# Performance work log

Measured on AMD Instinct MI355X. Metric: run time of the kernel, lower is better.

The kernel has to match this reference:

```python
import jax, jax.numpy as jnp
import numpy as np

MODEL_SIZE = 512
HEADS = 8
T = 2048
B = 2


def setup_inputs() -> dict:
    key = jax.random.key(0)
    ks = jax.random.split(key, 10)
    E = MODEL_SIZE
    w = 0.02  # weight init scale for numerical stability
    return {
        "input": jax.random.normal(ks[0], (T, B, E), jnp.float32),
        "pos": jax.random.normal(ks[1], (T, 1, E), jnp.float32),
        "in_proj_weight": jax.random.normal(ks[2], (3 * E, E), jnp.float32) * w,
        "out_proj_weight": jax.random.normal(ks[3], (E, E), jnp.float32) * w,
        "pos_proj_weight": jax.random.normal(ks[4], (E, E), jnp.float32) * w,
        "in_proj_bias": jax.random.normal(ks[5], (3 * E,), jnp.float32) * w,
        "out_proj_bias": jax.random.normal(ks[6], (E,), jnp.float32) * w,
        "pos_proj_bias": jax.random.normal(ks[7], (E,), jnp.float32) * w,
        "r_w_bias": jax.random.normal(ks[8], (HEADS, E // HEADS), jnp.float32) * w,
        "r_r_bias": jax.random.normal(ks[9], (HEADS, E // HEADS), jnp.float32) * w,
    }


def _rel_shift(x):
    # x: [B, H, T, R] -> Transformer-XL relative shift
    b, h, t, r = x.shape
    x = jnp.pad(x, ((0, 0), (0, 0), (0, 0), (1, 0)))  # [B,H,T,R+1]
    x = x.reshape(b, h, r + 1, t)[:, :, 1:, :]        # drop first row
    return x.reshape(b, h, t, r)


def reference(input, pos, in_proj_weight, out_proj_weight, pos_proj_weight,
              in_proj_bias, out_proj_bias, pos_proj_bias, r_w_bias, r_r_bias):
    t, b, e = input.shape
    h = r_w_bias.shape[0]
    d = e // h
    scale = 1.0 / np.sqrt(d).astype(np.float32)

    # fused QKV projection (time-first layout [T,B,E])
    qkv = input @ in_proj_weight.T + in_proj_bias          # [T,B,3E]
    q, k, v = jnp.split(qkv, 3, axis=-1)
    q = q.reshape(t, b, h, d)
    k = k.reshape(t, b, h, d)
    v = v.reshape(t, b, h, d)

    # relative position projection (pos batch dim is 1)
    r = (pos[:, 0] @ pos_proj_weight.T + pos_proj_bias).reshape(-1, h, d)  # [R,H,D]

    # content (AC) and position (BD) scores
    ac = jnp.einsum('tbhd,sbhd->bhts', q + r_w_bias, k)    # [B,H,T,T]
    bd = jnp.einsum('tbhd,rhd->bhtr', q + r_r_bias, r)     # [B,H,T,R]
    bd = _rel_shift(bd)[..., :t]

    attn = jax.nn.softmax((ac + bd) * scale, axis=-1)      # [B,H,T,T]
    ctx = jnp.einsum('bhts,sbhd->tbhd', attn, v).reshape(t, b, e)
    return ctx @ out_proj_weight.T + out_proj_bias
```

## Files before the change

kernel.cpp:

```cpp
#include <hip/hip_runtime.h>

#define T_SEQ 2048
#define BATCH 2
#define HEADS 8
#define DHEAD 64
#define EMB   512

typedef __attribute__((ext_vector_type(8))) short short8;
typedef __attribute__((ext_vector_type(4))) float floatx4;
typedef __attribute__((ext_vector_type(8))) unsigned short ushort8;
typedef __attribute__((ext_vector_type(4))) unsigned short ushort4v;

__device__ __forceinline__ unsigned short f2b(float f) {
    union { float f; unsigned u; } v; v.f = f;
    unsigned r = v.u + 0x7fffu + ((v.u >> 16) & 1u);
    return (unsigned short)(r >> 16);
}
__device__ __forceinline__ unsigned short f2bt(float f) {
    union { float f; unsigned u; } v; v.f = f;
    return (unsigned short)(v.u >> 16);
}
__device__ __forceinline__ float b2f(unsigned short s) {
    union { unsigned u; float f; } v; v.u = ((unsigned)s) << 16; return v.f;
}
__device__ __forceinline__ short8 ld_frag(const unsigned short* p) {
    ushort4v lo = *(const ushort4v*)p;
    ushort4v hi = *(const ushort4v*)(p + 4);
    short8 r;
    r[0] = lo[0]; r[1] = lo[1]; r[2] = lo[2]; r[3] = lo[3];
    r[4] = hi[0]; r[5] = hi[1]; r[6] = hi[2]; r[7] = hi[3];
    return r;
}
__device__ __forceinline__ void st8(unsigned short* p, ushort8 v) {
    ushort4v lo = { v[0], v[1], v[2], v[3] };
    ushort4v hi = { v[4], v[5], v[6], v[7] };
    *(ushort4v*)p = lo;
    *(ushort4v*)(p + 4) = hi;
}
#define MFMA16(a, b, c) __builtin_amdgcn_mfma_f32_16x16x32_bf16(a, b, c, 0, 0, 0)

__global__ __launch_bounds__(256)
void cvt_all(const float* __restrict__ s0, const float* __restrict__ s1,
             const float* __restrict__ s2, const float* __restrict__ s3,
             const float* __restrict__ s4,
             unsigned short* __restrict__ d0, unsigned short* __restrict__ d1,
             unsigned short* __restrict__ d2, unsigned short* __restrict__ d3,
             unsigned short* __restrict__ d4)
{
    const int i = blockIdx.x * 256 + threadIdx.x;
    const float* s; unsigned short* d; int off;
    if      (i <  524288) { s = s0; d = d0; off = i; }
    else if (i <  786432) { s = s1; d = d1; off = i -  524288; }
    else if (i <  983040) { s = s2; d = d2; off = i -  786432; }
    else if (i < 1048576) { s = s3; d = d3; off = i -  983040; }
    else if (i < 1114112) { s = s4; d = d4; off = i - 1048576; }
    else return;
    const float4 v = ((const float4*)s)[off];
    ushort4v o = { f2b(v.x), f2b(v.y), f2b(v.z), f2b(v.w) };
    ((ushort4v*)d)[off] = o;
}

template<int MODE>
__global__ __launch_bounds__(256)
void gemm_bf16(const unsigned short* __restrict__ A, const unsigned short* __restrict__ B,
               const float* __restrict__ bias, void* __restrict__ out0,
               void* __restrict__ out1, void* __restrict__ out2, int K)
{
    __shared__ unsigned short As[128 * 36];
    __shared__ unsigned short Bs[128 * 36];
    const int bm  = blockIdx.y * 128;
    const int bn  = blockIdx.x * 128;
    const int tid = threadIdx.x;
    const int lane = tid & 63, w = tid >> 6;
    const int m16 = lane & 15, quad = lane >> 4;
    const int wm = (w & 1) * 64, wn = (w >> 1) * 64;

    floatx4 acc[4][4];
    #pragma unroll
    for (int i = 0; i < 4; ++i)
        #pragma unroll
        for (int j = 0; j < 4; ++j) acc[i][j] = (floatx4){0.f, 0.f, 0.f, 0.f};

    for (int k0 = 0; k0 < K; k0 += 32) {
        #pragma unroll
        for (int s = tid; s < 512; s += 256) {
            const int row = s >> 2, c = (s & 3) * 8;
            *(ushort8*)&As[row * 36 + c] = *(const ushort8*)(A + (size_t)(bm + row) * K + k0 + c);
            *(ushort8*)&Bs[row * 36 + c] = *(const ushort8*)(B + (size_t)(bn + row) * K + k0 + c);
        }
        __syncthreads();
        short8 af[4], bf[4];
        #pragma unroll
        for (int f = 0; f < 4; ++f) {
            af[f] = ld_frag(&As[(wm + f * 16 + m16) * 36 + quad * 8]);
            bf[f] = ld_frag(&Bs[(wn + f * 16 + m16) * 36 + quad * 8]);
        }
        #pragma unroll
        for (int fm = 0; fm < 4; ++fm)
            #pragma unroll
            for (int fn = 0; fn < 4; ++fn)
                acc[fm][fn] = MFMA16(af[fm], bf[fn], acc[fm][fn]);
        __syncthreads();
    }

    #pragma unroll
    for (int fn = 0; fn < 4; ++fn) {
        const int n = bn + wn + fn * 16 + m16;
        const float bv = bias[n];
        #pragma unroll
        for (int fm = 0; fm < 4; ++fm) {
            #pragma unroll
            for (int rgi = 0; rgi < 4; ++rgi) {
                const int m = bm + wm + fm * 16 + quad * 4 + rgi;
                const float val = acc[fm][fn][rgi] + bv;
                if (MODE == 0) {
                    const int t = m >> 1, b = m & 1;
                    const int reg = n >> 9, c = n & 511, h = c >> 6, dd = c & 63;
                    unsigned short* dst = (unsigned short*)(reg == 0 ? out0 : (reg == 1 ? out1 : out2));
                    dst[((size_t)(b * HEADS + h) * T_SEQ + t) * DHEAD + dd] = f2b(val);
                } else if (MODE == 1) {
                    ((unsigned short*)out0)[(size_t)m * EMB + n] = f2b(val);
                } else {
                    ((float*)out0)[(size_t)m * EMB + n] = val;
                }
            }
        }
    }
}

__global__ __launch_bounds__(256)
void transpose_v(const unsigned short* __restrict__ v_s, unsigned short* __restrict__ vT)
{
    __shared__ unsigned short tile[64 * 68];
    const int t0 = blockIdx.x * 64, bh = blockIdx.y;
    const int tid = threadIdx.x;
    const unsigned short* src = v_s + ((size_t)bh * T_SEQ + t0) * DHEAD;
    #pragma unroll
    for (int s = tid; s < 512; s += 256) {
        const int row = s >> 3, c = (s & 7) * 8;
        st8(&tile[row * 68 + c], *(const ushort8*)(src + row * DHEAD + c));
    }
    __syncthreads();
    unsigned short* dst = vT + (size_t)bh * DHEAD * T_SEQ + t0;
    #pragma unroll
    for (int s = tid; s < 512; s += 256) {
        const int d = s >> 3, c = (s & 7) * 8;
        ushort8 o;
        #pragma unroll
        for (int j = 0; j < 8; ++j) o[j] = tile[(c + j) * 68 + d];
        *(ushort8*)(dst + (size_t)d * T_SEQ + c) = o;
    }
}

__global__ __launch_bounds__(256)
void attn_mfma(const unsigned short* __restrict__ qg_, const unsigned short* __restrict__ kg_,
               const unsigned short* __restrict__ vtg_, const unsigned short* __restrict__ rg_,
               const float* __restrict__ rwb, const float* __restrict__ rrb,
               unsigned short* __restrict__ ctx)
{
    const int T   = T_SEQ;
    const int tb  = blockIdx.x;
    const int t0  = tb * 64;
    const int bh  = blockIdx.y;
    const int h   = bh & 7;
    const int b   = bh >> 3;
    const int tid = threadIdx.x;
    const int lane = tid & 63;
    const int w    = tid >> 6;
    const int m16  = lane & 15;
    const int quad = lane >> 4;
    const int ibase = 16 * w + quad * 4;

    __shared__ unsigned short lds[34624];
    unsigned short* ring  = lds + 26112;
    unsigned short* qrw_s = lds;
    unsigned short* qrr_s = lds + 8704;

    const unsigned short* qg  = qg_  + ((size_t)bh * T + t0) * DHEAD;
    const unsigned short* kg  = kg_  + (size_t)bh * T * DHEAD;
    const unsigned short* vtg = vtg_ + (size_t)bh * DHEAD * T;
    const unsigned short* rg  = rg_  + h * DHEAD;

    const float QSCALE = 0.125f * 1.44269504089f;
    for (int idx = tid; idx < 65 * 16; idx += 256) {
        const int row = idx >> 4, c = (idx & 15) << 2;
        ushort4v qv = {0, 0, 0, 0};
        if (t0 + row < T) qv = *(const ushort4v*)(qg + row * DHEAD + c);
        const float4 rr = *(const float4*)(rrb + h * DHEAD + c);
        qrr_s[row * 68 + c + 0] = f2b((b2f(qv[0]) + rr.x) * QSCALE);
        qrr_s[row * 68 + c + 1] = f2b((b2f(qv[1]) + rr.y) * QSCALE);
        qrr_s[row * 68 + c + 2] = f2b((b2f(qv[2]) + rr.z) * QSCALE);
        qrr_s[row * 68 + c + 3] = f2b((b2f(qv[3]) + rr.w) * QSCALE);
        if (row < 64) {
            const float4 rw = *(const float4*)(rwb + h * DHEAD + c);
            qrw_s[row * 68 + c + 0] = f2b((b2f(qv[0]) + rw.x) * QSCALE);
            qrw_s[row * 68 + c + 1] = f2b((b2f(qv[1]) + rw.y) * QSCALE);
            qrw_s[row * 68 + c + 2] = f2b((b2f(qv[2]) + rw.z) * QSCALE);
            qrw_s[row * 68 + c + 3] = f2b((b2f(qv[3]) + rw.w) * QSCALE);
        }
    }
    __syncthreads();

    short8 a_ac[2], a_qrl[2], a_qru[2];
    {
        const unsigned short* p0 = &qrw_s[(16 * w + m16) * 68 + quad * 8];
        a_ac[0]  = ld_frag(p0);  a_ac[1]  = ld_frag(p0 + 32);
        const unsigned short* p1 = &qrr_s[(16 * w + m16) * 68 + quad * 8];
        a_qrl[0] = ld_frag(p1);  a_qrl[1] = ld_frag(p1 + 32);
        const unsigned short* p2 = &qrr_s[(16 * w + 1 + m16) * 68 + quad * 8];
        a_qru[0] = ld_frag(p2);  a_qru[1] = ld_frag(p2 + 32);
    }

    const int srow0 = tid >> 3,          scol0 = (tid & 7) * 8;
    const int srow1 = (tid + 256) >> 3,  scol1 = (tid & 7) * 8;

    ushort8 kr[2], vr[2], rr8[2];
    auto prefetch = [&](int s0n) {
        const bool ln = (s0n <= t0);
        const int jb = (ln ? (s0n + T - t0 - 64) : (s0n - t0 - 65)) + 64;
        int j0 = jb + srow0; j0 = j0 < 0 ? 0 : (j0 > T - 1 ? T - 1 : j0);
        int j1 = jb + srow1; j1 = j1 < 0 ? 0 : (j1 > T - 1 ? T - 1 : j1);
        kr[0]  = *(const ushort8*)(kg + (size_t)(s0n + srow0) * DHEAD + scol0);
        kr[1]  = *(const ushort8*)(kg + (size_t)(s0n + srow1) * DHEAD + scol1);
        vr[0]  = *(const ushort8*)(vtg + (size_t)srow0 * T + s0n + scol0);
        vr[1]  = *(const ushort8*)(vtg + (size_t)srow1 * T + s0n + scol1);
        rr8[0] = *(const ushort8*)(rg + (size_t)j0 * EMB + scol0);
        rr8[1] = *(const ushort8*)(rg + (size_t)j1 * EMB + scol1);
    };
    auto store_bufs = [&](int q) {
        unsigned short* kb = lds + q * 4352;
        unsigned short* vb = lds + 8704 + q * 4352;
        unsigned short* rb = lds + 17408 + q * 4352;
        st8(&kb[srow0 * 68 + scol0], kr[0]);
        st8(&kb[srow1 * 68 + scol1], kr[1]);
        st8(&vb[srow0 * 68 + scol0], vr[0]);
        st8(&vb[srow1 * 68 + scol1], vr[1]);
        st8(&rb[srow0 * 68 + scol0], rr8[0]);
        st8(&rb[srow1 * 68 + scol1], rr8[1]);
    };
    auto stage_to = [&](unsigned short* dstb, int jbase) {
        #pragma unroll
        for (int idx = tid; idx < 512; idx += 256) {
            const int row = idx >> 3, c = (idx & 7) * 8;
            int j = jbase + row; j = j < 0 ? 0 : (j > T - 1 ? T - 1 : j);
            st8(&dstb[row * 68 + c], *(const ushort8*)(rg + (size_t)j * EMB + c));
        }
    };
    auto qr_half = [&](const unsigned short* rsb, const short8* aq, int slotbase) {
        #pragma unroll
        for (int cc = 0; cc < 4; ++cc) {
            floatx4 q4 = (floatx4){0.f, 0.f, 0.f, 0.f};
            #pragma unroll
            for (int ks = 0; ks < 2; ++ks) {
                short8 bfr = ld_frag(&rsb[(16 * cc + m16) * 68 + ks * 32 + quad * 8]);
                q4 = MFMA16(aq[ks], bfr, q4);
            }
            #pragma unroll
            for (int rgi = 0; rgi < 4; ++rgi)
                ring[(ibase + rgi) * 133 + slotbase + 16 * cc + m16] = f2bt(q4[rgi]);
        }
    };

    floatx4 O[4];
    float lrun[4];
    #pragma unroll
    for (int ct = 0; ct < 4; ++ct) O[ct] = (floatx4){0.f, 0.f, 0.f, 0.f};
    #pragma unroll
    for (int rgi = 0; rgi < 4; ++rgi) lrun[rgi] = 0.f;

    {
        stage_to(lds + 17408 + 4352, T - t0 - 64);
        prefetch(0);
        __syncthreads();
        qr_half(lds + 17408 + 4352, a_qrl, 0);
        store_bufs(0);
        __syncthreads();
    }

    for (int na = 0; na < T / 64; ++na) {
        const int s0 = na * 64;
        const int p = na & 1;
        unsigned short* kb = lds + p * 4352;
        unsigned short* vb = lds + 8704 + p * 4352;
        unsigned short* rp = lds + 17408 + p * 4352;
        const bool lower = (s0 <= t0);
        const int nph    = lower ? (s0 >> 6) : ((s0 - t0) >> 6);
        const int rbase  = (nph & 1) * 64;
        const int wbase  = 64 - rbase;
        const bool hasNext = (na + 1 < T / 64);

        floatx4 acf[4];
        #pragma unroll
        for (int ct = 0; ct < 4; ++ct) {
            acf[ct] = (floatx4){0.f, 0.f, 0.f, 0.f};
            #pragma unroll
            for (int ks = 0; ks < 2; ++ks) {
                short8 bfr = ld_frag(&kb[(16 * ct + m16) * 68 + ks * 32 + quad * 8]);
                acf[ct] = MFMA16(a_ac[ks], bfr, acf[ct]);
            }
        }
        qr_half(rp, lower ? a_qrl : a_qru, wbase);
        if (hasNext) prefetch(s0 + 64);
        __syncthreads();

        if (s0 != t0) {
            #pragma unroll
            for (int ct = 0; ct < 4; ++ct) {
                #pragma unroll
                for (int rgi = 0; rgi < 4; ++rgi) {
                    const int i = ibase + rgi;
                    const int slot = ((63 - i + 16 * ct + m16) + rbase) & 127;
                    acf[ct][rgi] += b2f(ring[i * 133 + slot]);
                }
            }
            if (s0 == t0 + 64 && lane == 48 && w == 3)
                acf[0][3] -= b2f(ring[63 * 133 + (rbase & 127)]);
        } else {
            #pragma unroll
            for (int ct = 0; ct < 4; ++ct) {
                #pragma unroll
                for (int rgi = 0; rgi < 4; ++rgi) {
                    const int i = ibase + rgi, u = 16 * ct + m16;
                    if (u <= i) acf[ct][rgi] += b2f(ring[i * 133 + (((63 - i + u) + rbase) & 127)]);
                }
            }
            unsigned short* rpo = lds + 17408 + (1 - p) * 4352;
            __syncthreads();
            stage_to(rpo, -1);
            __syncthreads();
            qr_half(rpo, a_qru, 64);
            __syncthreads();
            #pragma unroll
            for (int ct = 0; ct < 4; ++ct) {
                #pragma unroll
                for (int rgi = 0; rgi < 4; ++rgi) {
                    const int i = ibase + rgi, u = 16 * ct + m16;
                    if (u >= i + 2) acf[ct][rgi] += b2f(ring[i * 133 + 63 - i + u]);
                }
            }
        }

        #pragma unroll
        for (int rgi = 0; rgi < 4; ++rgi) {
            #pragma unroll
            for (int ct = 0; ct < 4; ++ct) {
                const float pv = exp2f(acf[ct][rgi]);
                acf[ct][rgi] = pv;
                lrun[rgi] += pv;
            }
        }
        #pragma unroll
        for (int ct = 0; ct < 4; ++ct)
            #pragma unroll
            for (int rgi = 0; rgi < 4; ++rgi)
                rp[(ibase + rgi) * 68 + 16 * ct + m16] = f2bt(acf[ct][rgi]);
        if (hasNext) store_bufs(1 - p);
        __syncthreads();

        short8 ap[2];
        {
            const unsigned short* pp = &rp[(16 * w + m16) * 68 + quad * 8];
            ap[0] = ld_frag(pp); ap[1] = ld_frag(pp + 32);
        }
        #pragma unroll
        for (int ct = 0; ct < 4; ++ct) {
            #pragma unroll
            for (int ks = 0; ks < 2; ++ks) {
                short8 bfr = ld_frag(&vb[(16 * ct + m16) * 68 + ks * 32 + quad * 8]);
                O[ct] = MFMA16(ap[ks], bfr, O[ct]);
            }
        }
    }

    #pragma unroll
    for (int rgi = 0; rgi < 4; ++rgi) {
        float l = lrun[rgi];
        #pragma unroll
        for (int off = 1; off < 16; off <<= 1)
            l += __shfl_xor(l, off);
        const float inv = 1.f / l;
        const int t = t0 + ibase + rgi;
        #pragma unroll
        for (int ct = 0; ct < 4; ++ct)
            ctx[((size_t)t * BATCH + b) * EMB + h * DHEAD + 16 * ct + m16] = f2bt(O[ct][rgi] * inv);
    }
}

extern "C" void kernel_launch(void* const* d_in, const int* in_sizes, int n_in,
                              void* d_out, int out_size, void* d_ws, size_t ws_size,
                              hipStream_t stream)
{
    const float* input = (const float*)d_in[0];
    const float* pos   = (const float*)d_in[1];
    const float* w_in  = (const float*)d_in[2];
    const float* w_out = (const float*)d_in[3];
    const float* w_pos = (const float*)d_in[4];
    const float* b_in  = (const float*)d_in[5];
    const float* b_out = (const float*)d_in[6];
    const float* b_pos = (const float*)d_in[7];
    const float* rwb   = (const float*)d_in[8];
    const float* rrb   = (const float*)d_in[9];

    unsigned short* ws     = (unsigned short*)d_ws;
    unsigned short* inb    = ws;
    unsigned short* posb   = ws + 2097152;
    unsigned short* w_inb  = ws + 3145728;
    unsigned short* w_posb = ws + 3932160;
    unsigned short* v_s    = ws + 4194304;
    unsigned short* w_outb = ws + 6291456;
    unsigned short* q_s    = ws + 6553600;
    unsigned short* k_s    = ws + 8650752;
    unsigned short* vT     = ws + 10747904;
    unsigned short* r_b    = ws + 12845056;
    unsigned short* ctx_b  = ws + 13893632;

    cvt_all<<<4352, 256, 0, stream>>>(input, pos, w_in, w_pos, w_out,
                                      inb, posb, w_inb, w_posb, w_outb);
    gemm_bf16<0><<<dim3(12, 32), 256, 0, stream>>>(inb, w_inb, b_in, q_s, k_s, v_s, EMB);
    gemm_bf16<1><<<dim3(4, 16), 256, 0, stream>>>(posb, w_posb, b_pos, r_b, nullptr, nullptr, EMB);
    transpose_v<<<dim3(32, 16), 256, 0, stream>>>(v_s, vT);
    attn_mfma<<<dim3(32, 16), 256, 0, stream>>>(q_s, k_s, vT, r_b, rwb, rrb, ctx_b);
    gemm_bf16<2><<<dim3(4, 32), 256, 0, stream>>>(ctx_b, w_outb, b_out, d_out, nullptr, nullptr, EMB);
}
```

Baseline: 218.8 us.

## Fuse QKV and pos projections into one launch and transpose V in epilogue

Combines the QKV projection GEMM and the position projection GEMM into a single kernel launch, with the block index selecting the operands. The V slice is transposed through shared memory in the epilogue and written straight into the vT layout, which removes the separate transpose kernel and its global round trip. Both GEMMs now use a K-tile of 64 instead of 32, which halves the barrier count per output tile but doubles the shared memory per block and may lower occupancy.

New measurement: 205.0 us. 1.07x faster.

```diff
diff --git a/kernel.cpp b/kernel.cpp
--- a/kernel.cpp
+++ b/kernel.cpp
@@ -60,14 +60,129 @@
     ((ushort4v*)d)[off] = o;
 }
 
-template<int MODE>
 __global__ __launch_bounds__(256)
-void gemm_bf16(const unsigned short* __restrict__ A, const unsigned short* __restrict__ B,
-               const float* __restrict__ bias, void* __restrict__ out0,
-               void* __restrict__ out1, void* __restrict__ out2, int K)
+void gemm_qkv_pos(const unsigned short* __restrict__ inb, const unsigned short* __restrict__ w_inb,
+                  const float* __restrict__ b_in,
+                  const unsigned short* __restrict__ posb, const unsigned short* __restrict__ w_posb,
+                  const float* __restrict__ b_pos,
+                  unsigned short* __restrict__ q_s, unsigned short* __restrict__ k_s,
+                  unsigned short* __restrict__ vT, unsigned short* __restrict__ r_b)
 {
-    __shared__ unsigned short As[128 * 36];
-    __shared__ unsigned short Bs[128 * 36];
+    __shared__ unsigned short shmem[17408];
+    unsigned short* As = shmem;
+    unsigned short* Bs = shmem + 8704;
+    unsigned short* tb = shmem;
+
+    const int id = blockIdx.x;
+    const bool isPos = (id >= 384);
+    const int bx = isPos ? ((id - 384) & 3) : (id % 12);
+    const int by = isPos ? ((id - 384) >> 2) : (id / 12);
+    const unsigned short* A = isPos ? posb : inb;
+    const unsigned short* B = isPos ? w_posb : w_inb;
+    const float* bias = isPos ? b_pos : b_in;
+
+    const int bm  = by * 128;
+    const int bn  = bx * 128;
+    const int tid = threadIdx.x;
+    const int lane = tid & 63, w = tid >> 6;
+    const int m16 = lane & 15, quad = lane >> 4;
+    const int wm = (w & 1) * 64, wn = (w >> 1) * 64;
+
+    floatx4 acc[4][4];
+    #pragma unroll
+    for (int i = 0; i < 4; ++i)
+        #pragma unroll
+        for (int j = 0; j < 4; ++j) acc[i][j] = (floatx4){0.f, 0.f, 0.f, 0.f};
+
+    for (int k0 = 0; k0 < 512; k0 += 64) {
+        #pragma unroll
+        for (int s = tid; s < 1024; s += 256) {
+            const int row = s >> 3, c = (s & 7) * 8;
+            st8(&As[row * 68 + c], *(const ushort8*)(A + (size_t)(bm + row) * 512 + k0 + c));
+            st8(&Bs[row * 68 + c], *(const ushort8*)(B + (size_t)(bn + row) * 512 + k0 + c));
+        }
+        __syncthreads();
+        #pragma unroll
+        for (int ks = 0; ks < 2; ++ks) {
+            short8 af[4], bf[4];
+            #pragma unroll
+            for (int f = 0; f < 4; ++f) {
+                af[f] = ld_frag(&As[(wm + f * 16 + m16) * 68 + ks * 32 + quad * 8]);
+                bf[f] = ld_frag(&Bs[(wn + f * 16 + m16) * 68 + ks * 32 + quad * 8]);
+            }
+            #pragma unroll
+            for (int fm = 0; fm < 4; ++fm)
+                #pragma unroll
+                for (int fn = 0; fn < 4; ++fn)
+                    acc[fm][fn] = MFMA16(af[fm], bf[fn], acc[fm][fn]);
+        }
+        __syncthreads();
+    }
+
+    if (isPos) {
+        #pragma unroll
+        for (int fn = 0; fn < 4; ++fn) {
+            const int n = bn + wn + fn * 16 + m16;
+            const float bv = bias[n];
+            #pragma unroll
+            for (int fm = 0; fm < 4; ++fm)
+                #pragma unroll
+                for (int rgi = 0; rgi < 4; ++rgi) {
+                    const int m = bm + wm + fm * 16 + quad * 4 + rgi;
+                    r_b[(size_t)m * EMB + n] = f2b(acc[fm][fn][rgi] + bv);
+                }
+        }
+    } else if (bn < 1024) {
+        #pragma unroll
+        for (int fn = 0; fn < 4; ++fn) {
+            const int n = bn + wn + fn * 16 + m16;
+            const float bv = bias[n];
+            const int reg = n >> 9, c = n & 511, h = c >> 6, dd = c & 63;
+            unsigned short* dst = reg == 0 ? q_s : k_s;
+            #pragma unroll
+            for (int fm = 0; fm < 4; ++fm)
+                #pragma unroll
+                for (int rgi = 0; rgi < 4; ++rgi) {
+                    const int m = bm + wm + fm * 16 + quad * 4 + rgi;
+                    const int t = m >> 1, b = m & 1;
+                    dst[((size_t)(b * HEADS + h) * T_SEQ + t) * DHEAD + dd] = f2b(acc[fm][fn][rgi] + bv);
+                }
+        }
+    } else {
+        #pragma unroll
+        for (int fn = 0; fn < 4; ++fn) {
+            const int nl = wn + fn * 16 + m16;
+            const float bv = bias[bn + nl];
+            #pragma unroll
+            for (int fm = 0; fm < 4; ++fm)
+                #pragma unroll
+                for (int rgi = 0; rgi < 4; ++rgi) {
+                    const int ml = wm + fm * 16 + quad * 4 + rgi;
+                    tb[nl * 131 + ml] = f2b(acc[fm][fn][rgi] + bv);
+                }
+        }
+        __syncthreads();
+        const int t0g = bm >> 1;
+        for (int s2 = tid; s2 < 2048; s2 += 256) {
+            const int nl = s2 >> 4;
+            const int bsel = (s2 >> 3) & 1;
+            const int j = s2 & 7;
+            ushort8 o;
+            #pragma unroll
+            for (int k = 0; k < 8; ++k)
+                o[k] = tb[nl * 131 + ((j * 8 + k) * 2 + bsel)];
+            const int c = bn + nl - 1024, h = c >> 6, dd = c & 63;
+            *(ushort8*)(vT + ((size_t)(bsel * HEADS + h) * DHEAD + dd) * T_SEQ + t0g + j * 8) = o;
+        }
+    }
+}
+
+__global__ __launch_bounds__(256)
+void gemm_out(const unsigned short* __restrict__ A, const unsigned short* __restrict__ B,
+              const float* __restrict__ bias, float* __restrict__ out)
+{
+    __shared__ unsigned short As[128 * 68];
+    __shared__ unsigned short Bs[128 * 68];
     const int bm  = blockIdx.y * 128;
     const int bn  = blockIdx.x * 128;
     const int tid = threadIdx.x;
@@ -81,25 +196,28 @@
         #pragma unroll
         for (int j = 0; j < 4; ++j) acc[i][j] = (floatx4){0.f, 0.f, 0.f, 0.f};
 
-    for (int k0 = 0; k0 < K; k0 += 32) {
-        #pragma unroll
-        for (int s = tid; s < 512; s += 256) {
-            const int row = s >> 2, c = (s & 3) * 8;
-            *(ushort8*)&As[row * 36 + c] = *(const ushort8*)(A + (size_t)(bm + row) * K + k0 + c);
-            *(ushort8*)&Bs[row * 36 + c] = *(const ushort8*)(B + (size_t)(bn + row) * K + k0 + c);
-        }
-        __syncthreads();
-        short8 af[4], bf[4];
-        #pragma unroll
-        for (int f = 0; f < 4; ++f) {
-            af[f] = ld_frag(&As[(wm + f * 16 + m16) * 36 + quad * 8]);
-            bf[f] = ld_frag(&Bs[(wn + f * 16 + m16) * 36 + quad * 8]);
-        }
-        #pragma unroll
-        for (int fm = 0; fm < 4; ++fm)
-            #pragma unroll
-            for (int fn = 0; fn < 4; ++fn)
-                acc[fm][fn] = MFMA16(af[fm], bf[fn], acc[fm][fn]);
+    for (int k0 = 0; k0 < 512; k0 += 64) {
+        #pragma unroll
+        for (int s = tid; s < 1024; s += 256) {
+            const int row = s >> 3, c = (s & 7) * 8;
+            st8(&As[row * 68 + c], *(const ushort8*)(A + (size_t)(bm + row) * 512 + k0 + c));
+            st8(&Bs[row * 68 + c], *(const ushort8*)(B + (size_t)(bn + row) * 512 + k0 + c));
+        }
+        __syncthreads();
+        #pragma unroll
+        for (int ks = 0; ks < 2; ++ks) {
+            short8 af[4], bf[4];
+            #pragma unroll
+            for (int f = 0; f < 4; ++f) {
+                af[f] = ld_frag(&As[(wm + f * 16 + m16) * 68 + ks * 32 + quad * 8]);
+                bf[f] = ld_frag(&Bs[(wn + f * 16 + m16) * 68 + ks * 32 + quad * 8]);
+            }
+            #pragma unroll
+            for (int fm = 0; fm < 4; ++fm)
+                #pragma unroll
+                for (int fn = 0; fn < 4; ++fn)
+                    acc[fm][fn] = MFMA16(af[fm], bf[fn], acc[fm][fn]);
+        }
         __syncthreads();
     }
 
@@ -108,47 +226,12 @@
         const int n = bn + wn + fn * 16 + m16;
         const float bv = bias[n];
         #pragma unroll
-        for (int fm = 0; fm < 4; ++fm) {
+        for (int fm = 0; fm < 4; ++fm)
             #pragma unroll
             for (int rgi = 0; rgi < 4; ++rgi) {
                 const int m = bm + wm + fm * 16 + quad * 4 + rgi;
-                const float val = acc[fm][fn][rgi] + bv;
-                if (MODE == 0) {
-                    const int t = m >> 1, b = m & 1;
-                    const int reg = n >> 9, c = n & 511, h = c >> 6, dd = c & 63;
-                    unsigned short* dst = (unsigned short*)(reg == 0 ? out0 : (reg == 1 ? out1 : out2));
-                    dst[((size_t)(b * HEADS + h) * T_SEQ + t) * DHEAD + dd] = f2b(val);
-                } else if (MODE == 1) {
-                    ((unsigned short*)out0)[(size_t)m * EMB + n] = f2b(val);
-                } else {
-                    ((float*)out0)[(size_t)m * EMB + n] = val;
-                }
-            }
-        }
-    }
-}
-
-__global__ __launch_bounds__(256)
-void transpose_v(const unsigned short* __restrict__ v_s, unsigned short* __restrict__ vT)
-{
-    __shared__ unsigned short tile[64 * 68];
-    const int t0 = blockIdx.x * 64, bh = blockIdx.y;
-    const int tid = threadIdx.x;
-    const unsigned short* src = v_s + ((size_t)bh * T_SEQ + t0) * DHEAD;
-    #pragma unroll
-    for (int s = tid; s < 512; s += 256) {
-        const int row = s >> 3, c = (s & 7) * 8;
-        st8(&tile[row * 68 + c], *(const ushort8*)(src + row * DHEAD + c));
-    }
-    __syncthreads();
-    unsigned short* dst = vT + (size_t)bh * DHEAD * T_SEQ + t0;
-    #pragma unroll
-    for (int s = tid; s < 512; s += 256) {
-        const int d = s >> 3, c = (s & 7) * 8;
-        ushort8 o;
-        #pragma unroll
-        for (int j = 0; j < 8; ++j) o[j] = tile[(c + j) * 68 + d];
-        *(ushort8*)(dst + (size_t)d * T_SEQ + c) = o;
+                out[(size_t)m * EMB + n] = acc[fm][fn][rgi] + bv;
+            }
     }
 }
 
@@ -406,7 +489,6 @@
     unsigned short* posb   = ws + 2097152;
     unsigned short* w_inb  = ws + 3145728;
     unsigned short* w_posb = ws + 3932160;
-    unsigned short* v_s    = ws + 4194304;
     unsigned short* w_outb = ws + 6291456;
     unsigned short* q_s    = ws + 6553600;
     unsigned short* k_s    = ws + 8650752;
@@ -416,9 +498,8 @@
 
     cvt_all<<<4352, 256, 0, stream>>>(input, pos, w_in, w_pos, w_out,
                                       inb, posb, w_inb, w_posb, w_outb);
-    gemm_bf16<0><<<dim3(12, 32), 256, 0, stream>>>(inb, w_inb, b_in, q_s, k_s, v_s, EMB);
-    gemm_bf16<1><<<dim3(4, 16), 256, 0, stream>>>(posb, w_posb, b_pos, r_b, nullptr, nullptr, EMB);
-    transpose_v<<<dim3(32, 16), 256, 0, stream>>>(v_s, vT);
+    gemm_qkv_pos<<<448, 256, 0, stream>>>(inb, w_inb, b_in, posb, w_posb, b_pos,
+                                          q_s, k_s, vT, r_b);
     attn_mfma<<<dim3(32, 16), 256, 0, stream>>>(q_s, k_s, vT, r_b, rwb, rrb, ctx_b);
-    gemm_bf16<2><<<dim3(4, 32), 256, 0, stream>>>(ctx_b, w_outb, b_out, d_out, nullptr, nullptr, EMB);
-}
+    gemm_out<<<dim3(4, 32), 256, 0, stream>>>(ctx_b, w_outb, b_out, (float*)d_out);
+}
```
